# Kernel optimization log

Hardware: AMD Instinct MI355X
Metric: run time of the kernel (lower is better)

The kernel has to match this reference:

```python
import jax, jax.numpy as jnp
import numpy as np

T, B, H, D_MODEL = 4096, 16, 256, 256


def setup_inputs() -> dict:
    key = jax.random.key(0)
    ks = jax.random.split(key, 10)
    x = jax.random.normal(ks[0], (T, B, D_MODEL), jnp.float32)
    # episode-start (reset) flags, sparse
    starts = jax.random.bernoulli(ks[1], 0.005, (T, B, 1))
    state_re = jnp.zeros((1, B, H), jnp.float32)
    state_im = jnp.zeros((1, B, H), jnp.float32)
    # LRU parameterization: |Lambda| = exp(-exp(nu_log)) < 1 for any real nu_log
    nu_log = jax.random.uniform(ks[2], (H,), jnp.float32)
    theta_log = jax.random.uniform(ks[3], (H,), jnp.float32) * 2.0
    s_in = 1.0 / np.sqrt(D_MODEL).astype(np.float32)
    B_re = jax.random.normal(ks[4], (H, D_MODEL), jnp.float32) * s_in
    B_im = jax.random.normal(ks[5], (H, D_MODEL), jnp.float32) * s_in
    s_out = 1.0 / np.sqrt(H).astype(np.float32)
    C_re = jax.random.normal(ks[6], (D_MODEL, H), jnp.float32) * s_out
    C_im = jax.random.normal(ks[7], (D_MODEL, H), jnp.float32) * s_out
    D = jax.random.normal(ks[8], (D_MODEL,), jnp.float32)
    return dict(x=x, starts=starts, state_re=state_re, state_im=state_im,
                nu_log=nu_log, theta_log=theta_log, B_re=B_re, B_im=B_im,
                C_re=C_re, C_im=C_im, D=D)


def _cell_binary_op(lhs, rhs):
    # Resettable diagonal linear-recurrence combine (associative).
    (A_i, b_i), d_i = lhs
    (A_j, b_j), d_j = rhs
    A = jnp.where(d_j, A_j, A_j * A_i)
    b = jnp.where(d_j, b_j, A_j * b_i + b_j)
    return (A, b), jnp.logical_or(d_i, d_j)


def reference(x, starts, state_re, state_im, nu_log, theta_log,
              B_re, B_im, C_re, C_im, D):
    t, b = x.shape[0], x.shape[1]
    # cell.map_to_h
    Lam = jnp.exp(-jnp.exp(nu_log) + 1j * jnp.exp(theta_log))          # [H] complex
    gamma = jnp.sqrt(jnp.clip(1.0 - jnp.abs(Lam) ** 2, 1e-8))          # [H]
    Bu = (jnp.einsum('tbd,hd->tbh', x, B_re * gamma[:, None])
          + 1j * jnp.einsum('tbd,hd->tbh', x, B_im * gamma[:, None]))  # [T,B,H] c64
    Lam_el = jnp.broadcast_to(Lam, (t, b, H)).astype(jnp.complex64)

    # recurrent_associative_scan: prepend carry, scan, drop first element
    A0 = jnp.ones((1, b, H), jnp.complex64)
    b0 = (state_re + 1j * state_im).astype(jnp.complex64)
    d0 = jnp.zeros((1, b, 1), bool)
    A_all = jnp.concatenate([A0, Lam_el], axis=0)
    b_all = jnp.concatenate([b0, Bu], axis=0)
    d_all = jnp.concatenate([d0, starts], axis=0)
    (A_s, b_s), _ = jax.lax.associative_scan(
        _cell_binary_op, ((A_all, b_all), d_all), axis=0)
    h = b_s[1:]                                                        # [T,B,H] c64

    # cell.map_from_h: y = Re(C h) + D * x
    out = (jnp.einsum('tbh,dh->tbd', h.real, C_re)
           - jnp.einsum('tbh,dh->tbd', h.imag, C_im)
           + D * x)
    return out
```

## Files before the change

kernel.cpp:

```cpp
#include <hip/hip_runtime.h>
#include <hip/hip_bf16.h>

#define T_LEN 4096
#define BATCH 16
#define NH    256
#define DM    256
#define M_TOT (T_LEN * BATCH)

typedef __hip_bfloat16 bf16;
typedef __attribute__((ext_vector_type(8))) short bf16x8;
typedef __attribute__((ext_vector_type(4))) float f32x4;

__device__ __forceinline__ unsigned short f2bf_bits(float f) {
    unsigned int u = __float_as_uint(f);
    return (unsigned short)((u + 0x7fffu + ((u >> 16) & 1u)) >> 16);
}

__global__ __launch_bounds__(256) void prep_lam_kernel(
    const float* __restrict__ nu_log, const float* __restrict__ theta_log,
    float* __restrict__ lam , float* __restrict__ gam)
{
    int h = threadIdx.x;
    float nu  = nu_log[h];
    float th  = theta_log[h];
    float mod = expf(-expf(nu));
    float ang = expf(th);
    lam[h]      = mod * cosf(ang);
    lam[NH + h] = mod * sinf(ang);
    gam[h] = sqrtf(fmaxf(1.0f - mod * mod, 1e-8f));
}

__global__ __launch_bounds__(256) void prep_w_kernel(
    const float* __restrict__ B_re, const float* __restrict__ B_im,
    const float* __restrict__ C_re, const float* __restrict__ C_im,
    const float* __restrict__ gam,
    bf16* __restrict__ WaT, bf16* __restrict__ WcT)
{
    int idx = blockIdx.x * 256 + threadIdx.x;
    if (idx < 512 * 256) {
        int n = idx >> 8, k = idx & 255;
        int h = n >> 1;
        float v = ((n & 1) == 0 ? B_re[h * DM + k] : B_im[h * DM + k]) * gam[h];
        WaT[idx] = __float2bfloat16(v);
    } else {
        int j = idx - 512 * 256;
        int d = j >> 9, k = j & 511;
        int h = k >> 1;
        float v = ((k & 1) == 0) ? C_re[d * NH + h] : -C_im[d * NH + h];
        WcT[j] = __float2bfloat16(v);
    }
}

#define BM 128
#define BN 128
#define BK 32
#define LDK 40

template <typename TA, typename TC, bool SKIP>
__global__ __launch_bounds__(256) void mfma_gemm(
    const TA* __restrict__ A,
    const bf16* __restrict__ BT,
    TC* __restrict__ C,
    int M, int K, int N,
    const float* __restrict__ skip_x,
    const float* __restrict__ Dvec)
{
    __shared__ bf16 sA[BM * LDK];
    __shared__ bf16 sB[BN * LDK];

    const int tid  = threadIdx.x;
    const int lane = tid & 63;
    const int wid  = tid >> 6;
    const int m0 = blockIdx.y * BM;
    const int n0 = blockIdx.x * BN;
    const int tm = (wid >> 1) * 64;
    const int tn = (wid & 1) * 64;
    const int l15 = lane & 15;
    const int q   = lane >> 4;

    const int srow = tid >> 2;
    const int scol = (tid & 3) * 8;

    f32x4 zero4 = {0.f, 0.f, 0.f, 0.f};
    f32x4 acc[4][4];
    #pragma unroll
    for (int i = 0; i < 4; ++i)
        #pragma unroll
        for (int j = 0; j < 4; ++j) acc[i][j] = zero4;

    for (int k0 = 0; k0 < K; k0 += BK) {
        #pragma unroll
        for (int p = 0; p < 2; ++p) {
            int r = srow + p * 64;
            bf16 tmp[8];
            if constexpr (sizeof(TA) == 4) {
                const float* gp = (const float*)A + (size_t)(m0 + r) * K + k0 + scol;
                float4 v0 = *(const float4*)gp;
                float4 v1 = *(const float4*)(gp + 4);
                tmp[0] = __float2bfloat16(v0.x); tmp[1] = __float2bfloat16(v0.y);
                tmp[2] = __float2bfloat16(v0.z); tmp[3] = __float2bfloat16(v0.w);
                tmp[4] = __float2bfloat16(v1.x); tmp[5] = __float2bfloat16(v1.y);
                tmp[6] = __float2bfloat16(v1.z); tmp[7] = __float2bfloat16(v1.w);
            } else {
                *(int4*)tmp = *(const int4*)((const bf16*)A + (size_t)(m0 + r) * K + k0 + scol);
            }
            *(int4*)&sA[r * LDK + scol] = *(int4*)tmp;
            *(int4*)&sB[r * LDK + scol] =
                *(const int4*)(BT + (size_t)(n0 + r) * K + k0 + scol);
        }
        __syncthreads();

        bf16x8 af[4], bfr[4];
        #pragma unroll
        for (int i = 0; i < 4; ++i) {
            af[i]  = *(const bf16x8*)&sA[(tm + i * 16 + l15) * LDK + q * 8];
            bfr[i] = *(const bf16x8*)&sB[(tn + i * 16 + l15) * LDK + q * 8];
        }
        #pragma unroll
        for (int i = 0; i < 4; ++i)
            #pragma unroll
            for (int j = 0; j < 4; ++j)
                acc[i][j] = __builtin_amdgcn_mfma_f32_16x16x32_bf16(
                    af[i], bfr[j], acc[i][j], 0, 0, 0);
        __syncthreads();
    }

    #pragma unroll
    for (int i = 0; i < 4; ++i) {
        #pragma unroll
        for (int j = 0; j < 4; ++j) {
            #pragma unroll
            for (int r = 0; r < 4; ++r) {
                int row = m0 + tm + i * 16 + q * 4 + r;
                int col = n0 + tn + j * 16 + l15;
                float v = acc[i][j][r];
                if constexpr (SKIP) {
                    v += Dvec[col] * skip_x[(size_t)row * N + col];
                }
                if constexpr (sizeof(TC) == 4) {
                    ((float*)C)[(size_t)row * N + col] = v;
                } else {
                    ((bf16*)C)[(size_t)row * N + col] = __float2bfloat16(v);
                }
            }
        }
    }
}

#define SCHUNK 64
#define KHALO  32

__global__ __launch_bounds__(256) void scan_kernel(
    const bf16* __restrict__ Bu, const float* __restrict__ lam,
    const int* __restrict__ starts,
    const float* __restrict__ state_re, const float* __restrict__ state_im,
    bf16* __restrict__ H)
{
    int h = threadIdx.x;
    int b = blockIdx.x & (BATCH - 1);
    int c = blockIdx.x / BATCH;

    float lr = lam[h];
    float li = lam[NH + h];

    int t0 = c * SCHUNK;
    int tstart;
    float hre, him;
    if (c == 0) {
        tstart = 0;
        hre = state_re[b * NH + h];
        him = state_im[b * NH + h];
    } else {
        tstart = t0 - KHALO;
        hre = 0.0f; him = 0.0f;
    }
    int tend = t0 + SCHUNK;

    for (int t = tstart; t < tend; ++t) {
        size_t m = (size_t)t * BATCH + b;
        unsigned int v = *(const unsigned int*)(Bu + m * 512 + 2 * h);
        float br = __uint_as_float(v << 16);
        float bi = __uint_as_float(v & 0xffff0000u);
        bool st = (starts[t * BATCH + b] != 0);
        float nr = st ? br : fmaf(lr, hre, fmaf(-li, him, br));
        float ni = st ? bi : fmaf(lr, him, fmaf(li, hre, bi));
        hre = nr; him = ni;
        if (t >= t0) {
            unsigned int packed =
                ((unsigned int)f2bf_bits(him) << 16) | f2bf_bits(hre);
            *(unsigned int*)(H + m * 512 + 2 * h) = packed;
        }
    }
}

extern "C" void kernel_launch(void* const* d_in, const int* in_sizes, int n_in,
                              void* d_out, int out_size, void* d_ws, size_t ws_size,
                              hipStream_t stream)
{
    const float* x         = (const float*)d_in[0];
    const int*   starts    = (const int*)d_in[1];
    const float* state_re  = (const float*)d_in[2];
    const float* state_im  = (const float*)d_in[3];
    const float* nu_log    = (const float*)d_in[4];
    const float* theta_log = (const float*)d_in[5];
    const float* B_re      = (const float*)d_in[6];
    const float* B_im      = (const float*)d_in[7];
    const float* C_re      = (const float*)d_in[8];
    const float* C_im      = (const float*)d_in[9];
    const float* Dvec      = (const float*)d_in[10];
    float* out = (float*)d_out;

    char* ws = (char*)d_ws;
    float* lam = (float*)ws;
    float* gam = (float*)(ws + 2 * NH * sizeof(float));
    bf16*  WaT = (bf16*)(ws + 4096);
    bf16*  WcT = (bf16*)(ws + 4096 + 512 * 256 * 2);
    bf16*  Bu  = (bf16*)(ws + (1 << 20));
    bf16*  H   = (bf16*)(ws + (1 << 20) + (size_t)M_TOT * 512 * 2);

    prep_lam_kernel<<<1, 256, 0, stream>>>(nu_log, theta_log, lam, gam);
    prep_w_kernel<<<1024, 256, 0, stream>>>(B_re, B_im, C_re, C_im, gam, WaT, WcT);

    mfma_gemm<float, bf16, false>
        <<<dim3(512 / BN, M_TOT / BM), 256, 0, stream>>>(
        x, WaT, Bu, M_TOT, DM, 512, nullptr, nullptr);

    scan_kernel<<<(T_LEN / SCHUNK) * BATCH, 256, 0, stream>>>(
        Bu, lam, starts, state_re, state_im, H);

    mfma_gemm<bf16, float, true>
        <<<dim3(DM / BN, M_TOT / BM), 256, 0, stream>>>(
        H, WcT, out, M_TOT, 512, DM, x, Dvec);
}
```

Before: 263.6 us.

## Use direct global-to-LDS loads, XCD-aware tile mapping, pre-converted bf16 input, scan prefetch

Converts x to bf16 in a separate pass (staged in the output buffer) so both GEMMs load bf16 tiles via global_load_lds directly into unpadded LDS. Remaps 1D block ids so each XCD handles a contiguous range of M tiles, to improve L2 locality. Also prefetches the next Bu/starts value in the scan loop and hoists the D vector load out of the epilogue. Adds an extra conversion pass over x, and the unpadded LDS layout may cause bank conflicts.

Result: no change. 260.0 us (-1.4%).

```diff
diff --git a/kernel.cpp b/kernel.cpp
--- a/kernel.cpp
+++ b/kernel.cpp
@@ -14,6 +14,12 @@
 __device__ __forceinline__ unsigned short f2bf_bits(float f) {
     unsigned int u = __float_as_uint(f);
     return (unsigned short)((u + 0x7fffu + ((u >> 16) & 1u)) >> 16);
+}
+
+typedef const unsigned int __attribute__((address_space(1)))* gas_ptr;
+typedef unsigned int __attribute__((address_space(3)))* las_ptr;
+__device__ __forceinline__ void async16(const bf16* g, bf16* l) {
+    __builtin_amdgcn_global_load_lds((gas_ptr)g, (las_ptr)l, 16, 0, 0);
 }
 
 __global__ __launch_bounds__(256) void prep_lam_kernel(
@@ -51,70 +57,78 @@
     }
 }
 
-#define BM 128
-#define BN 128
-#define BK 32
-#define LDK 40
-
-template <typename TA, typename TC, bool SKIP>
+__global__ __launch_bounds__(256) void cvt_kernel(
+    const float* __restrict__ x, bf16* __restrict__ xb)
+{
+    size_t i = ((size_t)blockIdx.x * 256 + threadIdx.x) * 8;
+    float4 a = *(const float4*)(x + i);
+    float4 b = *(const float4*)(x + i + 4);
+    union { bf16 h[8]; int4 v; } u;
+    u.h[0] = __float2bfloat16(a.x); u.h[1] = __float2bfloat16(a.y);
+    u.h[2] = __float2bfloat16(a.z); u.h[3] = __float2bfloat16(a.w);
+    u.h[4] = __float2bfloat16(b.x); u.h[5] = __float2bfloat16(b.y);
+    u.h[6] = __float2bfloat16(b.z); u.h[7] = __float2bfloat16(b.w);
+    *(int4*)(xb + i) = u.v;
+}
+
+#define BKE 32
+
+template <typename TC, bool SKIP>
 __global__ __launch_bounds__(256) void mfma_gemm(
-    const TA* __restrict__ A,
+    const bf16* __restrict__ A,
     const bf16* __restrict__ BT,
     TC* __restrict__ C,
-    int M, int K, int N,
+    int K, int N,
+    int mpx,
+    int lnb,
     const float* __restrict__ skip_x,
     const float* __restrict__ Dvec)
 {
-    __shared__ bf16 sA[BM * LDK];
-    __shared__ bf16 sB[BN * LDK];
+    __shared__ bf16 sA[128 * BKE];
+    __shared__ bf16 sB[128 * BKE];
 
     const int tid  = threadIdx.x;
     const int lane = tid & 63;
     const int wid  = tid >> 6;
-    const int m0 = blockIdx.y * BM;
-    const int n0 = blockIdx.x * BN;
-    const int tm = (wid >> 1) * 64;
-    const int tn = (wid & 1) * 64;
+
+    const int bid = blockIdx.x;
+    const int xcd = bid & 7;
+    const int sl  = bid >> 3;
+    const int nt  = sl & ((1 << lnb) - 1);
+    const int mt  = xcd * mpx + (sl >> lnb);
+    const int m0  = mt * 128;
+    const int n0  = nt * 128;
+
+    const int tm  = (wid >> 1) * 64;
+    const int tn  = (wid & 1) * 64;
     const int l15 = lane & 15;
     const int q   = lane >> 4;
 
-    const int srow = tid >> 2;
-    const int scol = (tid & 3) * 8;
-
-    f32x4 zero4 = {0.f, 0.f, 0.f, 0.f};
+    const bf16* gA = A  + (size_t)(m0 + wid * 32 + (lane >> 2)) * K + (lane & 3) * 8;
+    const bf16* gB = BT + (size_t)(n0 + wid * 32 + (lane >> 2)) * K + (lane & 3) * 8;
+    const size_t rstep = (size_t)16 * K;
+    bf16* lA = sA + wid * 32 * BKE;
+    bf16* lB = sB + wid * 32 * BKE;
+
     f32x4 acc[4][4];
     #pragma unroll
     for (int i = 0; i < 4; ++i)
         #pragma unroll
-        for (int j = 0; j < 4; ++j) acc[i][j] = zero4;
-
-    for (int k0 = 0; k0 < K; k0 += BK) {
-        #pragma unroll
-        for (int p = 0; p < 2; ++p) {
-            int r = srow + p * 64;
-            bf16 tmp[8];
-            if constexpr (sizeof(TA) == 4) {
-                const float* gp = (const float*)A + (size_t)(m0 + r) * K + k0 + scol;
-                float4 v0 = *(const float4*)gp;
-                float4 v1 = *(const float4*)(gp + 4);
-                tmp[0] = __float2bfloat16(v0.x); tmp[1] = __float2bfloat16(v0.y);
-                tmp[2] = __float2bfloat16(v0.z); tmp[3] = __float2bfloat16(v0.w);
-                tmp[4] = __float2bfloat16(v1.x); tmp[5] = __float2bfloat16(v1.y);
-                tmp[6] = __float2bfloat16(v1.z); tmp[7] = __float2bfloat16(v1.w);
-            } else {
-                *(int4*)tmp = *(const int4*)((const bf16*)A + (size_t)(m0 + r) * K + k0 + scol);
-            }
-            *(int4*)&sA[r * LDK + scol] = *(int4*)tmp;
-            *(int4*)&sB[r * LDK + scol] =
-                *(const int4*)(BT + (size_t)(n0 + r) * K + k0 + scol);
-        }
+        for (int j = 0; j < 4; ++j) acc[i][j] = (f32x4){0.f, 0.f, 0.f, 0.f};
+
+    for (int k0 = 0; k0 < K; k0 += BKE) {
+        async16(gA,         lA);
+        async16(gA + rstep, lA + 16 * BKE);
+        async16(gB,         lB);
+        async16(gB + rstep, lB + 16 * BKE);
+        gA += BKE; gB += BKE;
         __syncthreads();
 
         bf16x8 af[4], bfr[4];
         #pragma unroll
         for (int i = 0; i < 4; ++i) {
-            af[i]  = *(const bf16x8*)&sA[(tm + i * 16 + l15) * LDK + q * 8];
-            bfr[i] = *(const bf16x8*)&sB[(tn + i * 16 + l15) * LDK + q * 8];
+            af[i]  = *(const bf16x8*)&sA[(tm + i * 16 + l15) * BKE + q * 8];
+            bfr[i] = *(const bf16x8*)&sB[(tn + i * 16 + l15) * BKE + q * 8];
         }
         #pragma unroll
         for (int i = 0; i < 4; ++i)
@@ -126,16 +140,17 @@
     }
 
     #pragma unroll
-    for (int i = 0; i < 4; ++i) {
-        #pragma unroll
-        for (int j = 0; j < 4; ++j) {
+    for (int j = 0; j < 4; ++j) {
+        int col = n0 + tn + j * 16 + l15;
+        float dv = SKIP ? Dvec[col] : 0.0f;
+        #pragma unroll
+        for (int i = 0; i < 4; ++i) {
             #pragma unroll
             for (int r = 0; r < 4; ++r) {
                 int row = m0 + tm + i * 16 + q * 4 + r;
-                int col = n0 + tn + j * 16 + l15;
                 float v = acc[i][j][r];
                 if constexpr (SKIP) {
-                    v += Dvec[col] * skip_x[(size_t)row * N + col];
+                    v += dv * skip_x[(size_t)row * N + col];
                 }
                 if constexpr (sizeof(TC) == 4) {
                     ((float*)C)[(size_t)row * N + col] = v;
@@ -176,20 +191,27 @@
     }
     int tend = t0 + SCHUNK;
 
+    unsigned int v = *(const unsigned int*)(Bu + ((size_t)tstart * BATCH + b) * 512 + 2 * h);
+    int st = starts[tstart * BATCH + b];
+
     for (int t = tstart; t < tend; ++t) {
-        size_t m = (size_t)t * BATCH + b;
-        unsigned int v = *(const unsigned int*)(Bu + m * 512 + 2 * h);
+        unsigned int vn = 0; int stn = 0;
+        if (t + 1 < tend) {
+            vn  = *(const unsigned int*)(Bu + ((size_t)(t + 1) * BATCH + b) * 512 + 2 * h);
+            stn = starts[(t + 1) * BATCH + b];
+        }
         float br = __uint_as_float(v << 16);
         float bi = __uint_as_float(v & 0xffff0000u);
-        bool st = (starts[t * BATCH + b] != 0);
         float nr = st ? br : fmaf(lr, hre, fmaf(-li, him, br));
         float ni = st ? bi : fmaf(lr, him, fmaf(li, hre, bi));
         hre = nr; him = ni;
         if (t >= t0) {
+            size_t m = (size_t)t * BATCH + b;
             unsigned int packed =
                 ((unsigned int)f2bf_bits(him) << 16) | f2bf_bits(hre);
             *(unsigned int*)(H + m * 512 + 2 * h) = packed;
         }
+        v = vn; st = stn;
     }
 }
 
@@ -217,18 +239,18 @@
     bf16*  WcT = (bf16*)(ws + 4096 + 512 * 256 * 2);
     bf16*  Bu  = (bf16*)(ws + (1 << 20));
     bf16*  H   = (bf16*)(ws + (1 << 20) + (size_t)M_TOT * 512 * 2);
+    bf16*  xb  = (bf16*)d_out;
 
     prep_lam_kernel<<<1, 256, 0, stream>>>(nu_log, theta_log, lam, gam);
     prep_w_kernel<<<1024, 256, 0, stream>>>(B_re, B_im, C_re, C_im, gam, WaT, WcT);
-
-    mfma_gemm<float, bf16, false>
-        <<<dim3(512 / BN, M_TOT / BM), 256, 0, stream>>>(
-        x, WaT, Bu, M_TOT, DM, 512, nullptr, nullptr);
+    cvt_kernel<<<M_TOT * DM / (256 * 8), 256, 0, stream>>>(x, xb);
+
+    mfma_gemm<bf16, false><<<2048, 256, 0, stream>>>(
+        xb, WaT, Bu, DM, 512, 64, 2, nullptr, nullptr);
 
     scan_kernel<<<(T_LEN / SCHUNK) * BATCH, 256, 0, stream>>>(
         Bu, lam, starts, state_re, state_im, H);
 
-    mfma_gemm<bf16, float, true>
-        <<<dim3(DM / BN, M_TOT / BM), 256, 0, stream>>>(
-        H, WcT, out, M_TOT, 512, DM, x, Dvec);
-}
+    mfma_gemm<float, true><<<1024, 256, 0, stream>>>(
+        H, WcT, out, 512, DM, 64, 1, x, Dvec);
+}
```
